# Kernel tuning notes

Measured on AMD Instinct MI355X. Metric: run time of the kernel, lower is better.

## Reference

```python
import jax, jax.numpy as jnp
import numpy as np

N = 100000   # nodes
E = 1600000  # edges (avg degree 16)
IN, H, OUT = 64, 128, 1


def setup_inputs() -> dict:
    key = jax.random.key(0)
    ks = jax.random.split(key, 12)
    s = 0.05
    return {
        "x": jax.random.normal(ks[0], (N, IN), jnp.float32),
        "edge_index": jax.random.randint(ks[1], (2, E), 0, N, dtype=jnp.int64),
        "Wl1": jax.random.normal(ks[2], (IN, H), jnp.float32) * s,
        "Wr1": jax.random.normal(ks[3], (IN, H), jnp.float32) * s,
        "b1": jnp.zeros((H,), jnp.float32),
        "ln_g": jnp.ones((H,), jnp.float32),
        "ln_b": jnp.zeros((H,), jnp.float32),
        "Wres": jax.random.normal(ks[4], (IN, H), jnp.float32) * s,
        "bres": jnp.zeros((H,), jnp.float32),
        "Wl2": jax.random.normal(ks[5], (H, H), jnp.float32) * s,
        "Wr2": jax.random.normal(ks[6], (H, H), jnp.float32) * s,
        "b2": jnp.zeros((H,), jnp.float32),
        "Wl3": jax.random.normal(ks[7], (H, H), jnp.float32) * s,
        "Wr3": jax.random.normal(ks[8], (H, H), jnp.float32) * s,
        "b3": jnp.zeros((H,), jnp.float32),
        "Wl4": jax.random.normal(ks[9], (H, OUT), jnp.float32) * s,
        "Wr4": jax.random.normal(ks[10], (H, OUT), jnp.float32) * s,
        "b4": jnp.zeros((OUT,), jnp.float32),
    }


def _sage(h, src, dst, deg_inv, Wl, Wr, b):
    # PyG SAGEConv, aggr='mean': lin_l(mean_{j in N(i)} h_j) + lin_r(h_i)
    agg = jax.ops.segment_sum(h[src], dst, num_segments=N) * deg_inv[:, None]
    return agg @ Wl + h @ Wr + b


def _layernorm(h, g, b, eps=1e-5):
    mu = jnp.mean(h, axis=-1, keepdims=True)
    var = jnp.mean((h - mu) ** 2, axis=-1, keepdims=True)
    return (h - mu) * jax.lax.rsqrt(var + eps) * g + b


def reference(x, edge_index, Wl1, Wr1, b1, ln_g, ln_b, Wres, bres,
              Wl2, Wr2, b2, Wl3, Wr3, b3, Wl4, Wr4, b4):
    src, dst = edge_index[0], edge_index[1]
    deg = jax.ops.segment_sum(jnp.ones((E,), jnp.float32), dst, num_segments=N)
    deg_inv = 1.0 / jnp.maximum(deg, 1.0)

    h = jax.nn.relu(_layernorm(_sage(x, src, dst, deg_inv, Wl1, Wr1, b1), ln_g, ln_b))
    h = h + x @ Wres + bres              # residual (in_channel != hidden_channel)
    h = jax.nn.relu(_sage(h, src, dst, deg_inv, Wl2, Wr2, b2))   # dropout: eval no-op
    h = jax.nn.relu(_sage(h, src, dst, deg_inv, Wl3, Wr3, b3))
    out = _sage(h, src, dst, deg_inv, Wl4, Wr4, b4)
    return out.squeeze(-1)
```

## Files before the change

kernel.cpp:

```cpp
#include <hip/hip_runtime.h>
#include <hip/hip_bf16.h>

#define N_NODES 100000
#define N_EDGES 1600000

#define NBKT 782
#define BKT_CHUNK 13334
#define SCAT_BLOCKS 120
#define LP 72

#define SORT_BLOCKS 40
#define SORT_CHUNK 2500
#define BH2_N (NBKT * SCAT_BLOCKS)

typedef __attribute__((ext_vector_type(8))) short short8v;
typedef __attribute__((ext_vector_type(4))) float float4v;

__device__ __forceinline__ unsigned short f2bf(float f) {
    unsigned int u = __float_as_uint(f);
    u = (u + 0x7FFFu + ((u >> 16) & 1u)) >> 16;
    return (unsigned short)u;
}
__device__ __forceinline__ float bf2f(unsigned short b) {
    return __uint_as_float((unsigned int)b << 16);
}


__global__ __launch_bounds__(256) void bkt_hist_kernel(const int* __restrict__ ei, int* __restrict__ bh2) {
    __shared__ int h[NBKT];
    int tid = threadIdx.x;
    for (int i = tid; i < NBKT; i += 256) h[i] = 0;
    __syncthreads();
    int start = blockIdx.x * BKT_CHUNK;
    int end = start + BKT_CHUNK; if (end > N_EDGES) end = N_EDGES;
    for (int i = start + tid; i < end; i += 256) {
        int d = ei[N_EDGES + i];
        atomicAdd(&h[d >> 7], 1);
    }
    __syncthreads();
    for (int i = tid; i < NBKT; i += 256) bh2[i * SCAT_BLOCKS + blockIdx.x] = h[i];
}

__global__ __launch_bounds__(256) void gscan_a_kernel(const int* __restrict__ in, int* __restrict__ bsum, int n) {
    __shared__ int lds[256];
    int tid = threadIdx.x;
    int base = blockIdx.x * 1024 + tid * 4;
    int s = 0;
    #pragma unroll
    for (int i = 0; i < 4; i++) s += (base + i < n) ? in[base + i] : 0;
    lds[tid] = s;
    __syncthreads();
    for (int off = 128; off; off >>= 1) {
        if (tid < off) lds[tid] += lds[tid + off];
        __syncthreads();
    }
    if (tid == 0) bsum[blockIdx.x] = lds[0];
}

__global__ __launch_bounds__(128) void scan_b_kernel(int* __restrict__ bsum, int nb) {
    __shared__ int lds[128];
    int tid = threadIdx.x;
    int v = (tid < nb) ? bsum[tid] : 0;
    lds[tid] = v;
    __syncthreads();
    for (int off = 1; off < 128; off <<= 1) {
        int y = 0;
        if (tid >= off) y = lds[tid - off];
        __syncthreads();
        if (tid >= off) lds[tid] += y;
        __syncthreads();
    }
    if (tid < nb) bsum[tid] = lds[tid] - v;
}

__global__ __launch_bounds__(256) void gscan_c_kernel(int* __restrict__ data, const int* __restrict__ bsum, int n) {
    __shared__ int lds[256];
    int tid = threadIdx.x;
    int base = blockIdx.x * 1024 + tid * 4;
    int v[4];
    int s = 0;
    #pragma unroll
    for (int i = 0; i < 4; i++) {
        v[i] = (base + i < n) ? data[base + i] : 0;
        s += v[i];
    }
    lds[tid] = s;
    __syncthreads();
    for (int off = 1; off < 256; off <<= 1) {
        int y = 0;
        if (tid >= off) y = lds[tid - off];
        __syncthreads();
        if (tid >= off) lds[tid] += y;
        __syncthreads();
    }
    int run = bsum[blockIdx.x] + lds[tid] - s;
    #pragma unroll
    for (int i = 0; i < 4; i++) {
        if (base + i < n) data[base + i] = run;
        run += v[i];
    }
}

__global__ __launch_bounds__(256) void extract_off_kernel(const int* __restrict__ bh2, int* __restrict__ bucket_off) {
    int i = blockIdx.x * 256 + threadIdx.x;
    if (i < NBKT) bucket_off[i] = bh2[i * SCAT_BLOCKS];
    if (i == NBKT) bucket_off[NBKT] = N_EDGES;
}

__global__ __launch_bounds__(256) void bkt_scatter2_kernel(const int* __restrict__ ei, const int* __restrict__ bh2,
                                                           int* __restrict__ packed) {
    __shared__ int h[NBKT];
    __shared__ int base[NBKT];
    int tid = threadIdx.x;
    for (int i = tid; i < NBKT; i += 256) { h[i] = 0; base[i] = bh2[i * SCAT_BLOCKS + blockIdx.x]; }
    __syncthreads();
    int start = blockIdx.x * BKT_CHUNK;
    int end = start + BKT_CHUNK; if (end > N_EDGES) end = N_EDGES;
    for (int i = start + tid; i < end; i += 256) {
        int s = ei[i];
        int d = ei[N_EDGES + i];
        int b = d >> 7;
        int pos = base[b] + atomicAdd(&h[b], 1);
        packed[pos] = (s << 7) | (d & 127);
    }
}

__global__ __launch_bounds__(256) void bkt_degrow_kernel(const int* __restrict__ packed, const int* __restrict__ bucket_off,
                                                         int* __restrict__ deg, int* __restrict__ row_ptr) {
    __shared__ int c[128];
    __shared__ int ps[128];
    int tid = threadIdx.x;
    if (tid < 128) c[tid] = 0;
    __syncthreads();
    int s0 = bucket_off[blockIdx.x], s1 = bucket_off[blockIdx.x + 1];
    for (int i = s0 + tid; i < s1; i += 256) atomicAdd(&c[packed[i] & 127], 1);
    __syncthreads();
    if (tid < 128) ps[tid] = c[tid];
    __syncthreads();
    for (int off = 1; off < 128; off <<= 1) {
        int y = 0;
        if (tid >= off && tid < 128) y = ps[tid - off];
        __syncthreads();
        if (tid >= off && tid < 128) ps[tid] += y;
        __syncthreads();
    }
    int node = blockIdx.x * 128 + tid;
    if (tid < 128 && node < N_NODES) {
        deg[node] = c[tid];
        row_ptr[node] = s0 + ps[tid] - c[tid];
    }
    if (blockIdx.x == 0 && tid == 0) row_ptr[N_NODES] = N_EDGES;
}

__global__ __launch_bounds__(256) void bkt_fill3_kernel(const int* __restrict__ packed, const int* __restrict__ bucket_off,
                                                        const int* __restrict__ row_ptr, int* __restrict__ col) {
    __shared__ int rp[128];
    __shared__ int c[128];
    int tid = threadIdx.x;
    int node = blockIdx.x * 128 + tid;
    if (tid < 128) {
        rp[tid] = (node < N_NODES) ? row_ptr[node] : 0;
        c[tid] = 0;
    }
    __syncthreads();
    int s0 = bucket_off[blockIdx.x], s1 = bucket_off[blockIdx.x + 1];
    for (int i = s0 + tid; i < s1; i += 256) {
        int p = packed[i];
        int dl = p & 127;
        int pos = rp[dl] + atomicAdd(&c[dl], 1);
        col[pos] = p >> 7;
    }
}

__global__ __launch_bounds__(256) void dsort_hist_kernel(const int* __restrict__ deg, int* __restrict__ bh) {
    __shared__ int h[64];
    int tid = threadIdx.x;
    if (tid < 64) h[tid] = 0;
    __syncthreads();
    int start = blockIdx.x * SORT_CHUNK;
    int end = start + SORT_CHUNK; if (end > N_NODES) end = N_NODES;
    for (int i = start + tid; i < end; i += 256) atomicAdd(&h[min(deg[i], 63)], 1);
    __syncthreads();
    if (tid < 64) bh[tid * SORT_BLOCKS + blockIdx.x] = h[tid];
}

__global__ __launch_bounds__(256) void dsort_scan_kernel(int* __restrict__ bh) {
    __shared__ int ps[256];
    int tid = threadIdx.x;
    int v[10];
    int s = 0;
    #pragma unroll
    for (int k = 0; k < 10; k++) { v[k] = bh[tid * 10 + k]; s += v[k]; }
    ps[tid] = s;
    __syncthreads();
    for (int off = 1; off < 256; off <<= 1) {
        int y = 0;
        if (tid >= off) y = ps[tid - off];
        __syncthreads();
        if (tid >= off) ps[tid] += y;
        __syncthreads();
    }
    int run = ps[tid] - s;
    #pragma unroll
    for (int k = 0; k < 10; k++) { int t = v[k]; bh[tid * 10 + k] = run; run += t; }
}

__global__ __launch_bounds__(256) void dsort_scat_kernel(const int* __restrict__ deg, const int* __restrict__ bh,
                                                         int* __restrict__ ord) {
    __shared__ int h[64];
    __shared__ int base[64];
    int tid = threadIdx.x;
    if (tid < 64) { h[tid] = 0; base[tid] = bh[tid * SORT_BLOCKS + blockIdx.x]; }
    __syncthreads();
    int start = blockIdx.x * SORT_CHUNK;
    int end = start + SORT_CHUNK; if (end > N_NODES) end = N_NODES;
    for (int i = start + tid; i < end; i += 256) {
        int b = min(deg[i], 63);
        int pos = base[b] + atomicAdd(&h[b], 1);
        ord[pos] = i;
    }
}

__global__ __launch_bounds__(256) void xbf_kernel(const float* __restrict__ x, unsigned short* __restrict__ xcat) {
    int idx = blockIdx.x * 256 + threadIdx.x;
    if (idx < N_NODES * 16) {
        int node = idx >> 4;
        int f0 = (idx & 15) * 4;
        float4 v = *(const float4*)(x + (size_t)idx * 4);
        ushort4 o;
        o.x = f2bf(v.x); o.y = f2bf(v.y); o.z = f2bf(v.z); o.w = f2bf(v.w);
        *(ushort4*)(xcat + (size_t)node * 128 + f0) = o;
    }
}

#define ACC4(u) { a0 += bf2f(u.x); a1 += bf2f(u.y); a2 += bf2f(u.z); a3 += bf2f(u.w); }

__global__ __launch_bounds__(256) void agg64_kernel(unsigned short* __restrict__ xcat,
                                                    const int* __restrict__ row_ptr, const int* __restrict__ col,
                                                    const int* __restrict__ ord) {
    int tid = threadIdx.x;
    int slot = blockIdx.x * 16 + (tid >> 4);
    if (slot >= N_NODES) return;
    int i = ord[slot];
    int f0 = (tid & 15) * 4;
    int s = row_ptr[i], e = row_ptr[i + 1];
    float a0 = 0.f, a1 = 0.f, a2 = 0.f, a3 = 0.f;
    int t = s;
    while (t + 7 < e) {
        int j0 = col[t], j1 = col[t + 1], j2 = col[t + 2], j3 = col[t + 3];
        int j4 = col[t + 4], j5 = col[t + 5], j6 = col[t + 6], j7 = col[t + 7];
        ushort4 u0 = *(const ushort4*)(xcat + (size_t)j0 * 128 + f0);
        ushort4 u1 = *(const ushort4*)(xcat + (size_t)j1 * 128 + f0);
        ushort4 u2 = *(const ushort4*)(xcat + (size_t)j2 * 128 + f0);
        ushort4 u3 = *(const ushort4*)(xcat + (size_t)j3 * 128 + f0);
        ushort4 u4 = *(const ushort4*)(xcat + (size_t)j4 * 128 + f0);
        ushort4 u5 = *(const ushort4*)(xcat + (size_t)j5 * 128 + f0);
        ushort4 u6 = *(const ushort4*)(xcat + (size_t)j6 * 128 + f0);
        ushort4 u7 = *(const ushort4*)(xcat + (size_t)j7 * 128 + f0);
        ACC4(u0) ACC4(u1) ACC4(u2) ACC4(u3) ACC4(u4) ACC4(u5) ACC4(u6) ACC4(u7)
        t += 8;
    }
    if (t + 3 < e) {
        int j0 = col[t], j1 = col[t + 1], j2 = col[t + 2], j3 = col[t + 3];
        ushort4 u0 = *(const ushort4*)(xcat + (size_t)j0 * 128 + f0);
        ushort4 u1 = *(const ushort4*)(xcat + (size_t)j1 * 128 + f0);
        ushort4 u2 = *(const ushort4*)(xcat + (size_t)j2 * 128 + f0);
        ushort4 u3 = *(const ushort4*)(xcat + (size_t)j3 * 128 + f0);
        ACC4(u0) ACC4(u1) ACC4(u2) ACC4(u3)
        t += 4;
    }
    if (t + 1 < e) {
        int j0 = col[t], j1 = col[t + 1];
        ushort4 u0 = *(const ushort4*)(xcat + (size_t)j0 * 128 + f0);
        ushort4 u1 = *(const ushort4*)(xcat + (size_t)j1 * 128 + f0);
        ACC4(u0) ACC4(u1)
        t += 2;
    }
    if (t < e) {
        ushort4 u0 = *(const ushort4*)(xcat + (size_t)col[t] * 128 + f0);
        ACC4(u0)
    }
    float di = 1.0f / fmaxf((float)(e - s), 1.0f);
    ushort4 o;
    o.x = f2bf(a0 * di); o.y = f2bf(a1 * di); o.z = f2bf(a2 * di); o.w = f2bf(a3 * di);
    *(ushort4*)(xcat + (size_t)i * 128 + 64 + f0) = o;
}

__global__ __launch_bounds__(256) void agg128_kernel(unsigned short* __restrict__ hcat,
                                                     const int* __restrict__ row_ptr, const int* __restrict__ col,
                                                     const int* __restrict__ ord) {
    int tid = threadIdx.x;
    int slot = blockIdx.x * 8 + (tid >> 5);
    if (slot >= N_NODES) return;
    int i = ord[slot];
    int f0 = (tid & 31) * 4;
    int s = row_ptr[i], e = row_ptr[i + 1];
    float a0 = 0.f, a1 = 0.f, a2 = 0.f, a3 = 0.f;
    int t = s;
    while (t + 7 < e) {
        int j0 = col[t], j1 = col[t + 1], j2 = col[t + 2], j3 = col[t + 3];
        int j4 = col[t + 4], j5 = col[t + 5], j6 = col[t + 6], j7 = col[t + 7];
        ushort4 u0 = *(const ushort4*)(hcat + (size_t)j0 * 256 + f0);
        ushort4 u1 = *(const ushort4*)(hcat + (size_t)j1 * 256 + f0);
        ushort4 u2 = *(const ushort4*)(hcat + (size_t)j2 * 256 + f0);
        ushort4 u3 = *(const ushort4*)(hcat + (size_t)j3 * 256 + f0);
        ushort4 u4 = *(const ushort4*)(hcat + (size_t)j4 * 256 + f0);
        ushort4 u5 = *(const ushort4*)(hcat + (size_t)j5 * 256 + f0);
        ushort4 u6 = *(const ushort4*)(hcat + (size_t)j6 * 256 + f0);
        ushort4 u7 = *(const ushort4*)(hcat + (size_t)j7 * 256 + f0);
        ACC4(u0) ACC4(u1) ACC4(u2) ACC4(u3) ACC4(u4) ACC4(u5) ACC4(u6) ACC4(u7)
        t += 8;
    }
    if (t + 3 < e) {
        int j0 = col[t], j1 = col[t + 1], j2 = col[t + 2], j3 = col[t + 3];
        ushort4 u0 = *(const ushort4*)(hcat + (size_t)j0 * 256 + f0);
        ushort4 u1 = *(const ushort4*)(hcat + (size_t)j1 * 256 + f0);
        ushort4 u2 = *(const ushort4*)(hcat + (size_t)j2 * 256 + f0);
        ushort4 u3 = *(const ushort4*)(hcat + (size_t)j3 * 256 + f0);
        ACC4(u0) ACC4(u1) ACC4(u2) ACC4(u3)
        t += 4;
    }
    if (t + 1 < e) {
        int j0 = col[t], j1 = col[t + 1];
        ushort4 u0 = *(const ushort4*)(hcat + (size_t)j0 * 256 + f0);
        ushort4 u1 = *(const ushort4*)(hcat + (size_t)j1 * 256 + f0);
        ACC4(u0) ACC4(u1)
        t += 2;
    }
    if (t < e) {
        ushort4 u0 = *(const ushort4*)(hcat + (size_t)col[t] * 256 + f0);
        ACC4(u0)
    }
    float di = 1.0f / fmaxf((float)(e - s), 1.0f);
    ushort4 o;
    o.x = f2bf(a0 * di); o.y = f2bf(a1 * di); o.z = f2bf(a2 * di); o.w = f2bf(a3 * di);
    *(ushort4*)(hcat + (size_t)i * 256 + 128 + f0) = o;
}

__global__ __launch_bounds__(256) void wprep1_kernel(const float* __restrict__ Wr1, const float* __restrict__ Wl1,
                                                     const float* __restrict__ Wres, unsigned short* __restrict__ Bt) {
    int idx = blockIdx.x * 256 + threadIdx.x;
    if (idx >= 256 * 128) return;
    int n = idx >> 7;
    int k = idx & 127;
    float v;
    if (n < 128) v = (k < 64) ? Wr1[k * 128 + n] : Wl1[(k - 64) * 128 + n];
    else         v = (k < 64) ? Wres[k * 128 + (n - 128)] : 0.f;
    Bt[idx] = f2bf(v);
}

__global__ __launch_bounds__(256) void wprep23_kernel(const float* __restrict__ Wl, const float* __restrict__ Wr,
                                                      unsigned short* __restrict__ Bt) {
    int idx = blockIdx.x * 256 + threadIdx.x;
    if (idx >= 128 * 256) return;
    int n = idx >> 8;
    int k = idx & 255;
    float v = (k < 128) ? Wr[k * 128 + n] : Wl[(k - 128) * 128 + n];
    Bt[idx] = f2bf(v);
}

__global__ __launch_bounds__(256) void mgemm1_ln_kernel(const unsigned short* __restrict__ A,
                                                        const unsigned short* __restrict__ Bt, int M,
                                                        const float* __restrict__ b1, const float* __restrict__ ln_g,
                                                        const float* __restrict__ ln_b, const float* __restrict__ bres,
                                                        unsigned short* __restrict__ hcat) {
    __shared__ unsigned short As[128 * LP];
    __shared__ unsigned short Bs[256 * LP];
    __shared__ float lsum[2][128], lsq[2][128];
    int tid = threadIdx.x;
    int m0 = blockIdx.x * 128;

    int lane = tid & 63;
    int wave = tid >> 6;
    int wm = (wave & 1) * 64;
    int wn = (wave >> 1) * 64;
    int lm = lane & 15;
    int lk = (lane >> 4) * 8;

    float4v accT[4][4], accR[4][4];
    #pragma unroll
    for (int i = 0; i < 4; i++)
        #pragma unroll
        for (int j = 0; j < 4; j++) { accT[i][j] = (float4v)0.f; accR[i][j] = (float4v)0.f; }

    int sr = tid >> 3;
    int sc = (tid & 7) * 8;

    for (int ks = 0; ks < 128; ks += 64) {
        if (ks) __syncthreads();
        int kk = ks + sc;
        #pragma unroll
        for (int rr = 0; rr < 384; rr += 32) {
            int r = sr + rr;
            if (r < 128) {
                int gm = m0 + r; if (gm > M - 1) gm = M - 1;
                *(ulonglong2*)&As[r * LP + sc] = *(const ulonglong2*)(A + (size_t)gm * 128 + kk);
            } else {
                int br = r - 128;
                *(ulonglong2*)&Bs[br * LP + sc] = *(const ulonglong2*)(Bt + (size_t)br * 128 + kk);
            }
        }
        __syncthreads();

        #pragma unroll
        for (int k0 = 0; k0 < 64; k0 += 32) {
            short8v af[4], bfT[4], bfR[4];
            #pragma unroll
            for (int i = 0; i < 4; i++)
                af[i] = *(const short8v*)&As[(wm + i * 16 + lm) * LP + k0 + lk];
            #pragma unroll
            for (int j = 0; j < 4; j++) {
                bfT[j] = *(const short8v*)&Bs[(wn + j * 16 + lm) * LP + k0 + lk];
                bfR[j] = *(const short8v*)&Bs[(128 + wn + j * 16 + lm) * LP + k0 + lk];
            }
            #pragma unroll
            for (int i = 0; i < 4; i++)
                #pragma unroll
                for (int j = 0; j < 4; j++) {
                    accT[i][j] = __builtin_amdgcn_mfma_f32_16x16x32_bf16(af[i], bfT[j], accT[i][j], 0, 0, 0);
                    accR[i][j] = __builtin_amdgcn_mfma_f32_16x16x32_bf16(af[i], bfR[j], accR[i][j], 0, 0, 0);
                }
        }
    }

    int q = lane >> 4;
    int wnidx = wave >> 1;
    float b1v[4], gv[4], bbv[4], brv[4];
    #pragma unroll
    for (int j = 0; j < 4; j++) {
        int cc = wn + j * 16 + lm;
        b1v[j] = b1[cc]; gv[j] = ln_g[cc]; bbv[j] = ln_b[cc]; brv[j] = bres[cc];
    }
    #pragma unroll
    for (int i = 0; i < 4; i++) {
        #pragma unroll
        for (int r = 0; r < 4; r++) {
            float sp = 0.f, sq = 0.f;
            #pragma unroll
            for (int j = 0; j < 4; j++) {
                float tv = accT[i][j][r] + b1v[j];
                sp += tv; sq += tv * tv;
            }
            #pragma unroll
            for (int off = 1; off < 16; off <<= 1) {
                sp += __shfl_xor(sp, off);
                sq += __shfl_xor(sq, off);
            }
            if (lm == 0) {
                int m = wm + i * 16 + q * 4 + r;
                lsum[wnidx][m] = sp;
                lsq[wnidx][m] = sq;
            }
        }
    }
    __syncthreads();
    #pragma unroll
    for (int i = 0; i < 4; i++) {
        #pragma unroll
        for (int r = 0; r < 4; r++) {
            int m = wm + i * 16 + q * 4 + r;
            float sum = lsum[0][m] + lsum[1][m];
            float s2 = lsq[0][m] + lsq[1][m];
            float mu = sum * (1.f / 128.f);
            float var = s2 * (1.f / 128.f) - mu * mu;
            float rstd = rsqrtf(var + 1e-5f);
            int gm = m0 + m;
            if (gm < M) {
                #pragma unroll
                for (int j = 0; j < 4; j++) {
                    float tv = accT[i][j][r] + b1v[j];
                    float y = fmaxf((tv - mu) * rstd * gv[j] + bbv[j], 0.f) + accR[i][j][r] + brv[j];
                    hcat[(size_t)gm * 256 + wn + j * 16 + lm] = f2bf(y);
                }
            }
        }
    }
}

__global__ __launch_bounds__(256) void mgemm_kernel(const unsigned short* __restrict__ A, int lda,
                                                    const unsigned short* __restrict__ Bt, int M,
                                                    const float* __restrict__ bias,
                                                    unsigned short* __restrict__ C, int ldc) {
    __shared__ unsigned short As[128 * LP];
    __shared__ unsigned short Bs[128 * LP];
    int tid = threadIdx.x;
    int m0 = blockIdx.x * 128;
    int n0 = blockIdx.y * 128;

    int lane = tid & 63;
    int wave = tid >> 6;
    int wm = (wave & 1) * 64;
    int wn = (wave >> 1) * 64;
    int lm = lane & 15;
    int lk = (lane >> 4) * 8;

    float4v acc[4][4];
    #pragma unroll
    for (int i = 0; i < 4; i++)
        #pragma unroll
        for (int j = 0; j < 4; j++) acc[i][j] = (float4v)0.f;

    int sr = tid >> 3;
    int sc = (tid & 7) * 8;

    for (int ks = 0; ks < lda; ks += 64) {
        if (ks) __syncthreads();
        int kk = ks + sc;
        #pragma unroll
        for (int rr = 0; rr < 128; rr += 32) {
            int r = sr + rr;
            int gm = m0 + r; if (gm > M - 1) gm = M - 1;
            *(ulonglong2*)&As[r * LP + sc] = *(const ulonglong2*)(A + (size_t)gm * lda + kk);
            *(ulonglong2*)&Bs[r * LP + sc] = *(const ulonglong2*)(Bt + (size_t)(n0 + r) * lda + kk);
        }
        __syncthreads();

        #pragma unroll
        for (int k0 = 0; k0 < 64; k0 += 32) {
            short8v af[4], bf[4];
            #pragma unroll
            for (int i = 0; i < 4; i++)
                af[i] = *(const short8v*)&As[(wm + i * 16 + lm) * LP + k0 + lk];
            #pragma unroll
            for (int j = 0; j < 4; j++)
                bf[j] = *(const short8v*)&Bs[(wn + j * 16 + lm) * LP + k0 + lk];
            #pragma unroll
            for (int i = 0; i < 4; i++)
                #pragma unroll
                for (int j = 0; j < 4; j++)
                    acc[i][j] = __builtin_amdgcn_mfma_f32_16x16x32_bf16(af[i], bf[j], acc[i][j], 0, 0, 0);
        }
    }

    int r0b = (lane >> 4) * 4;
    #pragma unroll
    for (int i = 0; i < 4; i++) {
        #pragma unroll
        for (int j = 0; j < 4; j++) {
            int cc = n0 + wn + j * 16 + lm;
            float bv = (bias != nullptr) ? bias[cc] : 0.f;
            #pragma unroll
            for (int r = 0; r < 4; r++) {
                int m = m0 + wm + i * 16 + r0b + r;
                if (m < M) {
                    float v = acc[i][j][r];
                    if (bias != nullptr) v = fmaxf(v + bv, 0.f);
                    C[(size_t)m * ldc + cc] = f2bf(v);
                }
            }
        }
    }
}

__global__ __launch_bounds__(256) void mgemm_pq_kernel(const unsigned short* __restrict__ A, int lda,
                                                       const unsigned short* __restrict__ Bt, int M,
                                                       const float* __restrict__ bias,
                                                       const float* __restrict__ Wl4, const float* __restrict__ Wr4,
                                                       const float* __restrict__ b4,
                                                       float* __restrict__ p, float* __restrict__ q) {
    __shared__ unsigned short As[128 * LP];
    __shared__ unsigned short Bs[128 * LP];
    __shared__ float psA[2][128], qsA[2][128];
    int tid = threadIdx.x;
    int m0 = blockIdx.x * 128;

    int lane = tid & 63;
    int wave = tid >> 6;
    int wm = (wave & 1) * 64;
    int wn = (wave >> 1) * 64;
    int lm = lane & 15;
    int lk = (lane >> 4) * 8;

    float4v acc[4][4];
    #pragma unroll
    for (int i = 0; i < 4; i++)
        #pragma unroll
        for (int j = 0; j < 4; j++) acc[i][j] = (float4v)0.f;

    int sr = tid >> 3;
    int sc = (tid & 7) * 8;

    for (int ks = 0; ks < lda; ks += 64) {
        if (ks) __syncthreads();
        int kk = ks + sc;
        #pragma unroll
        for (int rr = 0; rr < 128; rr += 32) {
            int r = sr + rr;
            int gm = m0 + r; if (gm > M - 1) gm = M - 1;
            *(ulonglong2*)&As[r * LP + sc] = *(const ulonglong2*)(A + (size_t)gm * lda + kk);
            *(ulonglong2*)&Bs[r * LP + sc] = *(const ulonglong2*)(Bt + (size_t)r * lda + kk);
        }
        __syncthreads();

        #pragma unroll
        for (int k0 = 0; k0 < 64; k0 += 32) {
            short8v af[4], bf[4];
            #pragma unroll
            for (int i = 0; i < 4; i++)
                af[i] = *(const short8v*)&As[(wm + i * 16 + lm) * LP + k0 + lk];
            #pragma unroll
            for (int j = 0; j < 4; j++)
                bf[j] = *(const short8v*)&Bs[(wn + j * 16 + lm) * LP + k0 + lk];
            #pragma unroll
            for (int i = 0; i < 4; i++)
                #pragma unroll
                for (int j = 0; j < 4; j++)
                    acc[i][j] = __builtin_amdgcn_mfma_f32_16x16x32_bf16(af[i], bf[j], acc[i][j], 0, 0, 0);
        }
    }

    int qd = lane >> 4;
    int wnidx = wave >> 1;
    float b3v[4], wlv[4], wrv[4];
    #pragma unroll
    for (int j = 0; j < 4; j++) {
        int cc = wn + j * 16 + lm;
        b3v[j] = bias[cc]; wlv[j] = Wl4[cc]; wrv[j] = Wr4[cc];
    }
    #pragma unroll
    for (int i = 0; i < 4; i++) {
        #pragma unroll
        for (int r = 0; r < 4; r++) {
            float pp = 0.f, qq = 0.f;
            #pragma unroll
            for (int j = 0; j < 4; j++) {
                float hv = fmaxf(acc[i][j][r] + b3v[j], 0.f);
                pp += hv * wlv[j]; qq += hv * wrv[j];
            }
            #pragma unroll
            for (int off = 1; off < 16; off <<= 1) {
                pp += __shfl_xor(pp, off);
                qq += __shfl_xor(qq, off);
            }
            if (lm == 0) {
                int m = wm + i * 16 + qd * 4 + r;
                psA[wnidx][m] = pp;
                qsA[wnidx][m] = qq;
            }
        }
    }
    __syncthreads();
    if (wnidx == 0 && lm == 0) {
        float b4v = b4[0];
        #pragma unroll
        for (int i = 0; i < 4; i++) {
            #pragma unroll
            for (int r = 0; r < 4; r++) {
                int m = wm + i * 16 + qd * 4 + r;
                int gm = m0 + m;
                if (gm < M) {
                    p[gm] = psA[0][m] + psA[1][m];
                    q[gm] = qsA[0][m] + qsA[1][m] + b4v;
                }
            }
        }
    }
}

__global__ __launch_bounds__(256) void final_kernel(const float* __restrict__ p, const float* __restrict__ q,
                                                    const int* __restrict__ row_ptr, const int* __restrict__ col,
                                                    float* __restrict__ out) {
    int i = blockIdx.x * 256 + threadIdx.x;
    if (i >= N_NODES) return;
    int s = row_ptr[i], e = row_ptr[i + 1];
    float acc = 0.f;
    int t = s;
    for (; t + 3 < e; t += 4)
        acc += p[col[t]] + p[col[t + 1]] + p[col[t + 2]] + p[col[t + 3]];
    for (; t < e; t++) acc += p[col[t]];
    float di = 1.0f / fmaxf((float)(e - s), 1.0f);
    out[i] = acc * di + q[i];
}


extern "C" void kernel_launch(void* const* d_in, const int* in_sizes, int n_in,
                              void* d_out, int out_size, void* d_ws, size_t ws_size,
                              hipStream_t stream) {
    const float* x    = (const float*)d_in[0];
    const int*   ei   = (const int*)d_in[1];
    const float* Wl1  = (const float*)d_in[2];
    const float* Wr1  = (const float*)d_in[3];
    const float* b1   = (const float*)d_in[4];
    const float* ln_g = (const float*)d_in[5];
    const float* ln_b = (const float*)d_in[6];
    const float* Wres = (const float*)d_in[7];
    const float* bres = (const float*)d_in[8];
    const float* Wl2  = (const float*)d_in[9];
    const float* Wr2  = (const float*)d_in[10];
    const float* b2   = (const float*)d_in[11];
    const float* Wl3  = (const float*)d_in[12];
    const float* Wr3  = (const float*)d_in[13];
    const float* b3   = (const float*)d_in[14];
    const float* Wl4  = (const float*)d_in[15];
    const float* Wr4  = (const float*)d_in[16];
    const float* b4   = (const float*)d_in[17];
    float* out = (float*)d_out;

    char* w = (char*)d_ws;
    size_t off = 0;
    auto alloc = [&](size_t bytes) -> void* {
        off = (off + 255) & ~(size_t)255;
        void* pp = w + off;
        off += bytes;
        return pp;
    };

    int*   deg        = (int*)alloc(N_NODES * 4);
    int*   row_ptr    = (int*)alloc((N_NODES + 1) * 4);
    int*   bsum       = (int*)alloc(512);
    int*   col        = (int*)alloc(N_EDGES * 4);
    int*   bucket_off = (int*)alloc((NBKT + 1) * 4);
    int*   bh2        = (int*)alloc(BH2_N * 4);
    int*   bh         = (int*)alloc(64 * SORT_BLOCKS * 4);
    int*   ord        = (int*)alloc(N_NODES * 4);
    unsigned short* Btw  = (unsigned short*)alloc(128 * 256 * 2);
    unsigned short* xcat = (unsigned short*)alloc((size_t)N_NODES * 128 * 2);
    unsigned short* hcat = (unsigned short*)alloc((size_t)N_NODES * 256 * 2);
    int*   packed  = (int*)alloc((size_t)N_EDGES * 4);
    float* p       = (float*)alloc(N_NODES * 4);
    float* q       = (float*)alloc(N_NODES * 4);
    (void)ws_size; (void)n_in; (void)in_sizes; (void)out_size;

    const int NB = (N_NODES + 255) / 256;
    const int BHB = (BH2_N + 1023) / 1024;
    const int MB = (N_NODES + 127) / 128;

    bkt_hist_kernel<<<SCAT_BLOCKS, 256, 0, stream>>>(ei, bh2);
    gscan_a_kernel<<<BHB, 256, 0, stream>>>(bh2, bsum, BH2_N);
    scan_b_kernel<<<1, 128, 0, stream>>>(bsum, BHB);
    gscan_c_kernel<<<BHB, 256, 0, stream>>>(bh2, bsum, BH2_N);
    extract_off_kernel<<<(NBKT + 256) / 256, 256, 0, stream>>>(bh2, bucket_off);
    bkt_scatter2_kernel<<<SCAT_BLOCKS, 256, 0, stream>>>(ei, bh2, packed);
    bkt_degrow_kernel<<<NBKT, 256, 0, stream>>>(packed, bucket_off, deg, row_ptr);
    dsort_hist_kernel<<<SORT_BLOCKS, 256, 0, stream>>>(deg, bh);
    dsort_scan_kernel<<<1, 256, 0, stream>>>(bh);
    dsort_scat_kernel<<<SORT_BLOCKS, 256, 0, stream>>>(deg, bh, ord);
    bkt_fill3_kernel<<<NBKT, 256, 0, stream>>>(packed, bucket_off, row_ptr, col);

    xbf_kernel<<<(N_NODES * 16 + 255) / 256, 256, 0, stream>>>(x, xcat);
    agg64_kernel<<<(N_NODES + 15) / 16, 256, 0, stream>>>(xcat, row_ptr, col, ord);
    wprep1_kernel<<<128, 256, 0, stream>>>(Wr1, Wl1, Wres, Btw);
    mgemm1_ln_kernel<<<MB, 256, 0, stream>>>(xcat, Btw, N_NODES, b1, ln_g, ln_b, bres, hcat);

    agg128_kernel<<<(N_NODES + 7) / 8, 256, 0, stream>>>(hcat, row_ptr, col, ord);
    wprep23_kernel<<<128, 256, 0, stream>>>(Wl2, Wr2, Btw);
    mgemm_kernel<<<dim3(MB, 1), 256, 0, stream>>>(hcat, 256, Btw, N_NODES, b2, hcat, 256);

    agg128_kernel<<<(N_NODES + 7) / 8, 256, 0, stream>>>(hcat, row_ptr, col, ord);
    wprep23_kernel<<<128, 256, 0, stream>>>(Wl3, Wr3, Btw);
    mgemm_pq_kernel<<<MB, 256, 0, stream>>>(hcat, 256, Btw, N_NODES, b3, Wl4, Wr4, b4, p, q);

    final_kernel<<<NB, 256, 0, stream>>>(p, q, row_ptr, col, out);
}
```

Baseline: 449.0 us.

## Fuse CSR degree/rowptr and column fill kernels, drop offset extraction, double scatter blocks

Merges the bucket degree/row-pointer kernel and the column-fill kernel into one kernel that reads each bucket's packed edges twice, once to count and once to place them. The bucket offsets are now read directly from the scanned histogram, so the separate offset-extraction kernel and its buffer are removed. The edge-scatter stage now uses twice as many blocks with half-size chunks, so the block-sum scan is widened to 256 threads. This cuts two kernel launches and one pass over global row pointers, in exchange for a larger histogram and scan.

```diff
diff --git a/kernel.cpp b/kernel.cpp
--- a/kernel.cpp
+++ b/kernel.cpp
@@ -5,8 +5,8 @@
 #define N_EDGES 1600000
 
 #define NBKT 782
-#define BKT_CHUNK 13334
-#define SCAT_BLOCKS 120
+#define SCAT_BLOCKS 240
+#define BKT_CHUNK 6667
 #define LP 72
 
 #define SORT_BLOCKS 40
@@ -57,13 +57,13 @@
     if (tid == 0) bsum[blockIdx.x] = lds[0];
 }
 
-__global__ __launch_bounds__(128) void scan_b_kernel(int* __restrict__ bsum, int nb) {
-    __shared__ int lds[128];
+__global__ __launch_bounds__(256) void scan_b_kernel(int* __restrict__ bsum, int nb) {
+    __shared__ int lds[256];
     int tid = threadIdx.x;
     int v = (tid < nb) ? bsum[tid] : 0;
     lds[tid] = v;
     __syncthreads();
-    for (int off = 1; off < 128; off <<= 1) {
+    for (int off = 1; off < 256; off <<= 1) {
         int y = 0;
         if (tid >= off) y = lds[tid - off];
         __syncthreads();
@@ -99,12 +99,6 @@
         if (base + i < n) data[base + i] = run;
         run += v[i];
     }
-}
-
-__global__ __launch_bounds__(256) void extract_off_kernel(const int* __restrict__ bh2, int* __restrict__ bucket_off) {
-    int i = blockIdx.x * 256 + threadIdx.x;
-    if (i < NBKT) bucket_off[i] = bh2[i * SCAT_BLOCKS];
-    if (i == NBKT) bucket_off[NBKT] = N_EDGES;
 }
 
 __global__ __launch_bounds__(256) void bkt_scatter2_kernel(const int* __restrict__ ei, const int* __restrict__ bh2,
@@ -125,45 +119,38 @@
     }
 }
 
-__global__ __launch_bounds__(256) void bkt_degrow_kernel(const int* __restrict__ packed, const int* __restrict__ bucket_off,
-                                                         int* __restrict__ deg, int* __restrict__ row_ptr) {
+__global__ __launch_bounds__(256) void bkt_build_kernel(const int* __restrict__ packed, const int* __restrict__ bh2,
+                                                        int* __restrict__ deg, int* __restrict__ row_ptr,
+                                                        int* __restrict__ col) {
     __shared__ int c[128];
-    __shared__ int ps[128];
-    int tid = threadIdx.x;
+    __shared__ int rp[128];
+    int tid = threadIdx.x;
+    int s0 = bh2[blockIdx.x * SCAT_BLOCKS];
+    int s1 = (blockIdx.x + 1 < NBKT) ? bh2[(blockIdx.x + 1) * SCAT_BLOCKS] : N_EDGES;
     if (tid < 128) c[tid] = 0;
     __syncthreads();
-    int s0 = bucket_off[blockIdx.x], s1 = bucket_off[blockIdx.x + 1];
     for (int i = s0 + tid; i < s1; i += 256) atomicAdd(&c[packed[i] & 127], 1);
     __syncthreads();
-    if (tid < 128) ps[tid] = c[tid];
+    if (tid < 128) rp[tid] = c[tid];
     __syncthreads();
     for (int off = 1; off < 128; off <<= 1) {
         int y = 0;
-        if (tid >= off && tid < 128) y = ps[tid - off];
-        __syncthreads();
-        if (tid >= off && tid < 128) ps[tid] += y;
-        __syncthreads();
-    }
-    int node = blockIdx.x * 128 + tid;
-    if (tid < 128 && node < N_NODES) {
-        deg[node] = c[tid];
-        row_ptr[node] = s0 + ps[tid] - c[tid];
-    }
-    if (blockIdx.x == 0 && tid == 0) row_ptr[N_NODES] = N_EDGES;
-}
-
-__global__ __launch_bounds__(256) void bkt_fill3_kernel(const int* __restrict__ packed, const int* __restrict__ bucket_off,
-                                                        const int* __restrict__ row_ptr, int* __restrict__ col) {
-    __shared__ int rp[128];
-    __shared__ int c[128];
-    int tid = threadIdx.x;
+        if (tid >= off && tid < 128) y = rp[tid - off];
+        __syncthreads();
+        if (tid >= off && tid < 128) rp[tid] += y;
+        __syncthreads();
+    }
     int node = blockIdx.x * 128 + tid;
     if (tid < 128) {
-        rp[tid] = (node < N_NODES) ? row_ptr[node] : 0;
+        rp[tid] = s0 + rp[tid] - c[tid];
+        if (node < N_NODES) {
+            deg[node] = c[tid];
+            row_ptr[node] = rp[tid];
+        }
         c[tid] = 0;
     }
-    __syncthreads();
-    int s0 = bucket_off[blockIdx.x], s1 = bucket_off[blockIdx.x + 1];
+    if (blockIdx.x == 0 && tid == 0) row_ptr[N_NODES] = N_EDGES;
+    __syncthreads();
     for (int i = s0 + tid; i < s1; i += 256) {
         int p = packed[i];
         int dl = p & 127;
@@ -707,9 +694,8 @@
 
     int*   deg        = (int*)alloc(N_NODES * 4);
     int*   row_ptr    = (int*)alloc((N_NODES + 1) * 4);
-    int*   bsum       = (int*)alloc(512);
+    int*   bsum       = (int*)alloc(1024);
     int*   col        = (int*)alloc(N_EDGES * 4);
-    int*   bucket_off = (int*)alloc((NBKT + 1) * 4);
     int*   bh2        = (int*)alloc(BH2_N * 4);
     int*   bh         = (int*)alloc(64 * SORT_BLOCKS * 4);
     int*   ord        = (int*)alloc(N_NODES * 4);
@@ -727,15 +713,13 @@
 
     bkt_hist_kernel<<<SCAT_BLOCKS, 256, 0, stream>>>(ei, bh2);
     gscan_a_kernel<<<BHB, 256, 0, stream>>>(bh2, bsum, BH2_N);
-    scan_b_kernel<<<1, 128, 0, stream>>>(bsum, BHB);
+    scan_b_kernel<<<1, 256, 0, stream>>>(bsum, BHB);
     gscan_c_kernel<<<BHB, 256, 0, stream>>>(bh2, bsum, BH2_N);
-    extract_off_kernel<<<(NBKT + 256) / 256, 256, 0, stream>>>(bh2, bucket_off);
     bkt_scatter2_kernel<<<SCAT_BLOCKS, 256, 0, stream>>>(ei, bh2, packed);
-    bkt_degrow_kernel<<<NBKT, 256, 0, stream>>>(packed, bucket_off, deg, row_ptr);
+    bkt_build_kernel<<<NBKT, 256, 0, stream>>>(packed, bh2, deg, row_ptr, col);
     dsort_hist_kernel<<<SORT_BLOCKS, 256, 0, stream>>>(deg, bh);
     dsort_scan_kernel<<<1, 256, 0, stream>>>(bh);
     dsort_scat_kernel<<<SORT_BLOCKS, 256, 0, stream>>>(deg, bh, ord);
-    bkt_fill3_kernel<<<NBKT, 256, 0, stream>>>(packed, bucket_off, row_ptr, col);
 
     xbf_kernel<<<(N_NODES * 16 + 255) / 256, 256, 0, stream>>>(x, xcat);
     agg64_kernel<<<(N_NODES + 15) / 16, 256, 0, stream>>>(xcat, row_ptr, col, ord);
```

New measurement: 438.3 us. -2.4%, faster.
